# Kernel tuning notes

Measured on AMD Instinct MI355X. Metric: run time of the kernel, lower is better.

## Reference

```python
import jax, jax.numpy as jnp
import numpy as np


def setup_inputs() -> dict:
    key = jax.random.key(0)
    k1, k2, k3, k4 = jax.random.split(key, 4)
    B, C, H, W = 8, 64, 64, 64
    Ck = C // 8  # query/key channels
    x = jax.random.normal(k1, (B, C, H, W), dtype=jnp.float32)
    # 1x1 conv1d weights (bias=False); spectral norm only rescales the weight,
    # so plain matrices are math-equivalent at a given parameter value.
    wq = jax.random.normal(k2, (Ck, C), dtype=jnp.float32) * (1.0 / np.sqrt(C))
    wk = jax.random.normal(k3, (Ck, C), dtype=jnp.float32) * (1.0 / np.sqrt(C))
    wv = jax.random.normal(k4, (C, C), dtype=jnp.float32) * (1.0 / np.sqrt(C))
    gamma = jnp.array([0.5], dtype=jnp.float32)  # nonzero so attention path is exercised
    return {"x": x, "wq": wq, "wk": wk, "wv": wv, "gamma": gamma}


def reference(x, wq, wk, wv, gamma):
    B, C, H, W = x.shape
    xf = x.reshape(B, C, H * W)                      # [B, C, N]
    f = jnp.einsum('kc,bcn->bkn', wq, xf)            # [B, C/8, N]
    g = jnp.einsum('kc,bcn->bkn', wk, xf)            # [B, C/8, N]
    h = jnp.einsum('oc,bcn->bon', wv, xf)            # [B, C,   N]
    scores = jnp.einsum('bkn,bkm->bnm', f, g)        # f^T g, [B, N, N]
    beta = jax.nn.softmax(scores, axis=1)            # softmax over dim=1 (rows), as in torch
    o = jnp.einsum('bcn,bnm->bcm', h, beta)          # [B, C, N]
    out = gamma[0] * o + xf
    return out.reshape(B, C, H, W)
```

## Files before the change

### kernel.cpp

```cpp
#include <hip/hip_runtime.h>
#include <hip/hip_bf16.h>

typedef __bf16 bf16x8 __attribute__((ext_vector_type(8)));
typedef float f32x4 __attribute__((ext_vector_type(4)));
typedef float f32x16 __attribute__((ext_vector_type(16)));
typedef unsigned int uint2v __attribute__((ext_vector_type(2)));

#define MFMA16 __builtin_amdgcn_mfma_f32_16x16x32_bf16
#define MFMA32 __builtin_amdgcn_mfma_f32_32x32x16_bf16

__device__ __forceinline__ unsigned short f2b(float f) {
  unsigned int u = __float_as_uint(f);
  u += 0x7FFFu + ((u >> 16) & 1u);
  return (unsigned short)(u >> 16);
}

__device__ __forceinline__ float b2f(unsigned short s) {
  return __uint_as_float(((unsigned)s) << 16);
}

union U128 {
  uint4 u;
  unsigned short s[8];
  bf16x8 b;
};

union BPack {
  __hip_bfloat162 h2;
  unsigned u;
};

__device__ __forceinline__ unsigned packbf(float a, float b) {
  BPack p;
  p.h2 = __float22bfloat162_rn(make_float2(a, b));
  return p.u;
}

__global__ __launch_bounds__(256, 2) void proj_kernel(
    const float* __restrict__ x, const float* __restrict__ wq,
    const float* __restrict__ wk, const float* __restrict__ wv_w,
    unsigned short* __restrict__ f_t, unsigned short* __restrict__ g_t,
    unsigned short* __restrict__ h_out) {
  __shared__ unsigned short xT[64 * 64];
  __shared__ unsigned short wT[96 * 72];
  __shared__ unsigned short hT[64 * 72];

  const int tid = (int)threadIdx.x;
  const int wvp = tid >> 6;
  const int lane = tid & 63;
  const int b = (int)blockIdx.x & 7;
  const int n0 = ((int)blockIdx.x >> 3) << 6;

  {
    const float* xb = x + ((size_t)b << 18) + n0 + lane;
    const int c0 = wvp * 16;
    float xv[16];
#pragma unroll
    for (int cc = 0; cc < 16; ++cc) xv[cc] = xb[(size_t)(c0 + cc) << 12];
#pragma unroll
    for (int p = 0; p < 4; ++p) {
      const int c = c0 + 4 * p;
      uint2 d;
      d.x = packbf(xv[4 * p + 0], xv[4 * p + 1]);
      d.y = packbf(xv[4 * p + 2], xv[4 * p + 3]);
      const int g = c >> 3;
      const int idx = lane * 64 + (((g ^ (lane & 7)) << 3) | (((c >> 2) & 1) << 2));
      *(uint2*)&xT[idx] = d;
    }
  }
#pragma unroll
  for (int i = 0; i < 20; ++i) {
    const int idx = i * 256 + tid;
    const float wval = (idx < 512) ? wq[idx] * 1.44269504f
                     : (idx < 1024) ? wk[idx - 512]
                                    : wv_w[idx - 1024];
    wT[(idx >> 6) * 72 + (idx & 63)] = f2b(wval);
  }
  __syncthreads();

  const int t = lane & 15, q = lane >> 4;
  const int nloc = wvp * 16 + t;
  U128 Bf[2];
#pragma unroll
  for (int kp = 0; kp < 2; ++kp) {
    const int g = kp * 4 + q;
    Bf[kp].u = *(const uint4*)&xT[nloc * 64 + ((g ^ (nloc & 7)) << 3)];
  }
  const int nabs = n0 + nloc;

  {
    f32x4 acc = {0.f, 0.f, 0.f, 0.f};
#pragma unroll
    for (int kp = 0; kp < 2; ++kp) {
      U128 Af;
      Af.u = *(const uint4*)&wT[t * 72 + ((kp * 4 + q) << 3)];
      acc = MFMA16(Af.b, Bf[kp].b, acc, 0, 0, 0);
    }
    uint2 d;
    d.x = packbf(acc[0], acc[1]);
    d.y = packbf(acc[2], acc[3]);
    unsigned short* dst = (q & 2) ? g_t : f_t;
    *(uint2*)&dst[((size_t)((b << 12) + nabs) << 3) + ((q & 1) << 2)] = d;
  }
#pragma unroll
  for (int rt = 1; rt < 5; ++rt) {
    f32x4 acc = {0.f, 0.f, 0.f, 0.f};
#pragma unroll
    for (int kp = 0; kp < 2; ++kp) {
      U128 Af;
      Af.u = *(const uint4*)&wT[(rt * 16 + t) * 72 + ((kp * 4 + q) << 3)];
      acc = MFMA16(Af.b, Bf[kp].b, acc, 0, 0, 0);
    }
    const int cbase = (rt - 1) * 16 + 4 * q;
#pragma unroll
    for (int reg = 0; reg < 4; ++reg)
      hT[(cbase + reg) * 72 + nloc] = f2b(acc[reg]);
  }
  __syncthreads();

  {
    const int hc = tid & 63;
    const int hw = tid >> 6;
    const uint4 v0 = *(const uint4*)&hT[hc * 72 + hw * 16];
    const uint4 v1 = *(const uint4*)&hT[hc * 72 + hw * 16 + 8];
    const size_t hbase =
        ((size_t)b << 18) + ((size_t)((n0 + hw * 16) >> 3) << 9) + (hc << 3);
    *(uint4*)&h_out[hbase] = v0;
    *(uint4*)&h_out[hbase + 512] = v1;
  }
}

__global__ __launch_bounds__(256, 2) void attn_kernel(
    const unsigned short* __restrict__ f_t, const unsigned short* __restrict__ g_t,
    const unsigned short* __restrict__ h, const float* __restrict__ x,
    const float* __restrict__ gamma, float* __restrict__ out) {
  __shared__ unsigned short Opart[4][32][66];
  __shared__ float lred[4][64];
  __shared__ float lsum[64];

  const int tid = (int)threadIdx.x;
  const int wave = tid >> 6;
  const int lane = tid & 63;
  const int ml = lane & 31;
  const int hh = lane >> 5;

  const int b = (int)blockIdx.x & 7;
  const int m0 = ((int)blockIdx.x >> 3) << 6;

  const unsigned short* fb = f_t + ((size_t)b << 15);
  const unsigned short* hb = h + ((size_t)b << 18);

  U128 G0, G1;
  G0.u = make_uint4(0u, 0u, 0u, 0u);
  G1.u = make_uint4(0u, 0u, 0u, 0u);
  if (hh == 0) {
    G0.u = *(const uint4*)(g_t + ((size_t)((b << 12) + m0 + ml) << 3));
    G1.u = *(const uint4*)(g_t + ((size_t)((b << 12) + m0 + 32 + ml) << 3));
  }

  f32x16 O00 = {}, O01 = {}, O10 = {}, O11 = {};
  float2 lp0v = make_float2(0.f, 0.f), lp1v = make_float2(0.f, 0.f);
  const f32x16 ZC = {};

  const int nbase = wave << 10;

  const unsigned short* fp = fb + ((size_t)(nbase + ml) << 3);
  const unsigned short* hp = hb + ((nbase >> 3) << 9) + (hh << 9) + (ml << 3);

  U128 F0, F1, Ha_e[4], Ha_o[4];
  f32x16 S0, S1;

  F0.u = *(const uint4*)(fp);
  F1.u = *(const uint4*)(fp + 256);
  Ha_e[0].u = *(const uint4*)(hp);
  Ha_e[1].u = *(const uint4*)(hp + 256);
  Ha_e[2].u = *(const uint4*)(hp + 1024);
  Ha_e[3].u = *(const uint4*)(hp + 1280);
  S0 = MFMA32(F0.b, G0.b, ZC, 0, 0, 0);
  S1 = MFMA32(F0.b, G1.b, ZC, 0, 0, 0);

  auto half = [&](f32x16& S, const U128& G, float2& lp, f32x16& Oa, f32x16& Ob,
                  const U128* Hv, const U128& Fn, bool produce) {
    float e[16];
#pragma unroll
    for (int r = 0; r < 16; ++r) e[r] = __builtin_amdgcn_exp2f(S[r]);
    if (produce) S = MFMA32(Fn.b, G.b, ZC, 0, 0, 0);
    lp.x += ((e[0] + e[2]) + (e[4] + e[6])) + ((e[8] + e[10]) + (e[12] + e[14]));
    lp.y += ((e[1] + e[3]) + (e[5] + e[7])) + ((e[9] + e[11]) + (e[13] + e[15]));
#pragma unroll
    for (int kt = 0; kt < 2; ++kt) {
      const unsigned A0 = packbf(e[8 * kt + 0], e[8 * kt + 1]);
      const unsigned A1 = packbf(e[8 * kt + 2], e[8 * kt + 3]);
      const unsigned B0 = packbf(e[8 * kt + 4], e[8 * kt + 5]);
      const unsigned B1 = packbf(e[8 * kt + 6], e[8 * kt + 7]);
      const uint2v r0 = __builtin_amdgcn_permlane32_swap(A0, B0, false, false);
      const uint2v r1 = __builtin_amdgcn_permlane32_swap(A1, B1, false, false);
      U128 P;
      P.u.x = r0[0];
      P.u.y = r1[0];
      P.u.z = r0[1];
      P.u.w = r1[1];
      Oa = MFMA32(Hv[2 * kt + 0].b, P.b, Oa, 0, 0, 0);
      Ob = MFMA32(Hv[2 * kt + 1].b, P.b, Ob, 0, 0, 0);
    }
  };
  auto body = [&](const U128* Hv, const U128& Fn, bool produce) {
    half(S0, G0, lp0v, O00, O01, Hv, Fn, produce);
    half(S1, G1, lp1v, O10, O11, Hv, Fn, produce);
  };

#pragma unroll 1
  for (int j = 0; j < 15; ++j) {
    Ha_o[0].u = *(const uint4*)(hp + 2048);
    Ha_o[1].u = *(const uint4*)(hp + 2304);
    Ha_o[2].u = *(const uint4*)(hp + 3072);
    Ha_o[3].u = *(const uint4*)(hp + 3328);
    F0.u = *(const uint4*)(fp + 512);
    body(Ha_e, F1, true);
    hp += 4096;
    Ha_e[0].u = *(const uint4*)(hp);
    Ha_e[1].u = *(const uint4*)(hp + 256);
    Ha_e[2].u = *(const uint4*)(hp + 1024);
    Ha_e[3].u = *(const uint4*)(hp + 1280);
    F1.u = *(const uint4*)(fp + 768);
    body(Ha_o, F0, true);
    fp += 512;
  }
  Ha_o[0].u = *(const uint4*)(hp + 2048);
  Ha_o[1].u = *(const uint4*)(hp + 2304);
  Ha_o[2].u = *(const uint4*)(hp + 3072);
  Ha_o[3].u = *(const uint4*)(hp + 3328);
  body(Ha_e, F1, true);
  body(Ha_o, F1, false);

  float lp0 = lp0v.x + lp0v.y;
  float lp1 = lp1v.x + lp1v.y;
  lp0 += __shfl_xor(lp0, 32, 64);
  lp1 += __shfl_xor(lp1, 32, 64);
  if (hh == 0) {
    lred[wave][ml] = lp0;
    lred[wave][32 + ml] = lp1;
  }

  const float gam = gamma[0];

  auto stash = [&](const f32x16& Oa, const f32x16& Ob) {
#pragma unroll
    for (int r = 0; r < 8; ++r) {
      const int c0 = ((2 * r) & 3) + 8 * (r >> 1) + 4 * hh;
      *(unsigned*)&Opart[wave][ml][c0] = packbf(Oa[2 * r], Oa[2 * r + 1]);
      *(unsigned*)&Opart[wave][ml][c0 + 32] = packbf(Ob[2 * r], Ob[2 * r + 1]);
    }
  };
  auto drain = [&](int p) {
    const int c = tid >> 2;
    const int m8 = (tid & 3) << 3;
    float a[8];
#pragma unroll
    for (int j = 0; j < 8; ++j) a[j] = 0.f;
#pragma unroll
    for (int w = 0; w < 4; ++w)
#pragma unroll
      for (int j = 0; j < 8; ++j) a[j] += b2f(Opart[w][m8 + j][c]);
    const f32x4 l0 = *(const f32x4*)&lsum[p * 32 + m8];
    const f32x4 l1 = *(const f32x4*)&lsum[p * 32 + m8 + 4];
    const size_t oi = (((size_t)b * 64 + c) << 12) + m0 + p * 32 + m8;
    f32x4 xo0 = *(const f32x4*)(x + oi);
    f32x4 xo1 = *(const f32x4*)(x + oi + 4);
#pragma unroll
    for (int j = 0; j < 4; ++j) {
      xo0[j] += gam / l0[j] * a[j];
      xo1[j] += gam / l1[j] * a[j + 4];
    }
    *(f32x4*)(out + oi) = xo0;
    *(f32x4*)(out + oi + 4) = xo1;
  };

  stash(O00, O01);
  __syncthreads();
  if (tid < 64)
    lsum[tid] = (lred[0][tid] + lred[1][tid]) + (lred[2][tid] + lred[3][tid]);
  __syncthreads();
  drain(0);
  __syncthreads();
  stash(O10, O11);
  __syncthreads();
  drain(1);
}

extern "C" void kernel_launch(void* const* d_in, const int* in_sizes, int n_in,
                              void* d_out, int out_size, void* d_ws, size_t ws_size,
                              hipStream_t stream) {
  (void)in_sizes; (void)n_in; (void)out_size; (void)ws_size;
  const float* x = (const float*)d_in[0];
  const float* wq = (const float*)d_in[1];
  const float* wk = (const float*)d_in[2];
  const float* wv = (const float*)d_in[3];
  const float* gamma = (const float*)d_in[4];
  float* out = (float*)d_out;

  unsigned short* f_t = (unsigned short*)d_ws;
  unsigned short* g_t = f_t + (size_t)8 * 4096 * 8;
  unsigned short* h = g_t + (size_t)8 * 4096 * 8;

  proj_kernel<<<512, 256, 0, stream>>>(x, wq, wk, wv, f_t, g_t, h);
  attn_kernel<<<512, 256, 0, stream>>>(f_t, g_t, h, x, gamma, out);
}
```

Before: 100.5 us.

## Fuse projection and attention kernels with a software grid barrier

Merges the projection kernel and the attention kernel into one persistent launch. A global atomic-counter barrier, reset by a memset before launch, separates the two phases, and the shared memory of both phases is overlaid through a union. This removes the second kernel launch and its inter-kernel gap. It relies on all 512 blocks being co-resident, which needs 2 blocks per CU on 256 CUs, and the spin-wait has a guard that could let blocks proceed early and read stale data. It also adds a memset call.

```diff
diff --git a/kernel.cpp b/kernel.cpp
--- a/kernel.cpp
+++ b/kernel.cpp
@@ -36,256 +36,285 @@
   return p.u;
 }
 
-__global__ __launch_bounds__(256, 2) void proj_kernel(
+__device__ __forceinline__ void grid_barrier(unsigned* bar, unsigned nblk) {
+  __syncthreads();
+  if (threadIdx.x == 0) {
+    __threadfence();
+    atomicAdd(bar, 1u);
+    unsigned v;
+    int guard = 0;
+    do {
+      v = __hip_atomic_load(bar, __ATOMIC_RELAXED, __HIP_MEMORY_SCOPE_AGENT);
+    } while (v < nblk && ++guard < (1 << 27));
+    __threadfence();
+  }
+  __syncthreads();
+}
+
+__global__ __launch_bounds__(256, 2) void fused_kernel(
     const float* __restrict__ x, const float* __restrict__ wq,
     const float* __restrict__ wk, const float* __restrict__ wv_w,
     unsigned short* __restrict__ f_t, unsigned short* __restrict__ g_t,
-    unsigned short* __restrict__ h_out) {
-  __shared__ unsigned short xT[64 * 64];
-  __shared__ unsigned short wT[96 * 72];
-  __shared__ unsigned short hT[64 * 72];
+    unsigned short* __restrict__ h, const float* __restrict__ gamma,
+    float* __restrict__ out, unsigned* __restrict__ bar) {
+  __shared__ union SMem {
+    struct {
+      unsigned short xT[64 * 64];
+      unsigned short wT[96 * 72];
+      unsigned short hT[64 * 72];
+    } p;
+    struct {
+      unsigned short Opart[4][32][66];
+      float lred[4][64];
+      float lsum[64];
+    } a;
+  } sm;
 
   const int tid = (int)threadIdx.x;
-  const int wvp = tid >> 6;
-  const int lane = tid & 63;
   const int b = (int)blockIdx.x & 7;
-  const int n0 = ((int)blockIdx.x >> 3) << 6;
+  const int t64 = (int)blockIdx.x >> 3;
 
   {
-    const float* xb = x + ((size_t)b << 18) + n0 + lane;
-    const int c0 = wvp * 16;
-    float xv[16];
-#pragma unroll
-    for (int cc = 0; cc < 16; ++cc) xv[cc] = xb[(size_t)(c0 + cc) << 12];
-#pragma unroll
-    for (int p = 0; p < 4; ++p) {
-      const int c = c0 + 4 * p;
+    const int wvp = tid >> 6;
+    const int lane = tid & 63;
+    const int n0 = t64 << 6;
+
+    {
+      const float* xb = x + ((size_t)b << 18) + n0 + lane;
+      const int c0 = wvp * 16;
+      float xv[16];
+#pragma unroll
+      for (int cc = 0; cc < 16; ++cc) xv[cc] = xb[(size_t)(c0 + cc) << 12];
+#pragma unroll
+      for (int p = 0; p < 4; ++p) {
+        const int c = c0 + 4 * p;
+        uint2 d;
+        d.x = packbf(xv[4 * p + 0], xv[4 * p + 1]);
+        d.y = packbf(xv[4 * p + 2], xv[4 * p + 3]);
+        const int g = c >> 3;
+        const int idx =
+            lane * 64 + (((g ^ (lane & 7)) << 3) | (((c >> 2) & 1) << 2));
+        *(uint2*)&sm.p.xT[idx] = d;
+      }
+    }
+#pragma unroll
+    for (int i = 0; i < 20; ++i) {
+      const int idx = i * 256 + tid;
+      const float wval = (idx < 512) ? wq[idx] * 1.44269504f
+                       : (idx < 1024) ? wk[idx - 512]
+                                      : wv_w[idx - 1024];
+      sm.p.wT[(idx >> 6) * 72 + (idx & 63)] = f2b(wval);
+    }
+    __syncthreads();
+
+    const int t = lane & 15, q = lane >> 4;
+    const int nloc = wvp * 16 + t;
+    U128 Bf[2];
+#pragma unroll
+    for (int kp = 0; kp < 2; ++kp) {
+      const int g = kp * 4 + q;
+      Bf[kp].u = *(const uint4*)&sm.p.xT[nloc * 64 + ((g ^ (nloc & 7)) << 3)];
+    }
+    const int nabs = n0 + nloc;
+
+    {
+      f32x4 acc = {0.f, 0.f, 0.f, 0.f};
+#pragma unroll
+      for (int kp = 0; kp < 2; ++kp) {
+        U128 Af;
+        Af.u = *(const uint4*)&sm.p.wT[t * 72 + ((kp * 4 + q) << 3)];
+        acc = MFMA16(Af.b, Bf[kp].b, acc, 0, 0, 0);
+      }
       uint2 d;
-      d.x = packbf(xv[4 * p + 0], xv[4 * p + 1]);
-      d.y = packbf(xv[4 * p + 2], xv[4 * p + 3]);
-      const int g = c >> 3;
-      const int idx = lane * 64 + (((g ^ (lane & 7)) << 3) | (((c >> 2) & 1) << 2));
-      *(uint2*)&xT[idx] = d;
+      d.x = packbf(acc[0], acc[1]);
+      d.y = packbf(acc[2], acc[3]);
+      unsigned short* dst = (q & 2) ? g_t : f_t;
+      *(uint2*)&dst[((size_t)((b << 12) + nabs) << 3) + ((q & 1) << 2)] = d;
+    }
+#pragma unroll
+    for (int rt = 1; rt < 5; ++rt) {
+      f32x4 acc = {0.f, 0.f, 0.f, 0.f};
+#pragma unroll
+      for (int kp = 0; kp < 2; ++kp) {
+        U128 Af;
+        Af.u = *(const uint4*)&sm.p.wT[(rt * 16 + t) * 72 + ((kp * 4 + q) << 3)];
+        acc = MFMA16(Af.b, Bf[kp].b, acc, 0, 0, 0);
+      }
+      const int cbase = (rt - 1) * 16 + 4 * q;
+#pragma unroll
+      for (int reg = 0; reg < 4; ++reg)
+        sm.p.hT[(cbase + reg) * 72 + nloc] = f2b(acc[reg]);
+    }
+    __syncthreads();
+
+    {
+      const int hc = tid & 63;
+      const int hw = tid >> 6;
+      const uint4 v0 = *(const uint4*)&sm.p.hT[hc * 72 + hw * 16];
+      const uint4 v1 = *(const uint4*)&sm.p.hT[hc * 72 + hw * 16 + 8];
+      const size_t hbase =
+          ((size_t)b << 18) + ((size_t)((n0 + hw * 16) >> 3) << 9) + (hc << 3);
+      *(uint4*)&h[hbase] = v0;
+      *(uint4*)&h[hbase + 512] = v1;
     }
   }
-#pragma unroll
-  for (int i = 0; i < 20; ++i) {
-    const int idx = i * 256 + tid;
-    const float wval = (idx < 512) ? wq[idx] * 1.44269504f
-                     : (idx < 1024) ? wk[idx - 512]
-                                    : wv_w[idx - 1024];
-    wT[(idx >> 6) * 72 + (idx & 63)] = f2b(wval);
-  }
-  __syncthreads();
-
-  const int t = lane & 15, q = lane >> 4;
-  const int nloc = wvp * 16 + t;
-  U128 Bf[2];
-#pragma unroll
-  for (int kp = 0; kp < 2; ++kp) {
-    const int g = kp * 4 + q;
-    Bf[kp].u = *(const uint4*)&xT[nloc * 64 + ((g ^ (nloc & 7)) << 3)];
-  }
-  const int nabs = n0 + nloc;
+
+  grid_barrier(bar, (unsigned)gridDim.x);
 
   {
-    f32x4 acc = {0.f, 0.f, 0.f, 0.f};
-#pragma unroll
-    for (int kp = 0; kp < 2; ++kp) {
-      U128 Af;
-      Af.u = *(const uint4*)&wT[t * 72 + ((kp * 4 + q) << 3)];
-      acc = MFMA16(Af.b, Bf[kp].b, acc, 0, 0, 0);
-    }
-    uint2 d;
-    d.x = packbf(acc[0], acc[1]);
-    d.y = packbf(acc[2], acc[3]);
-    unsigned short* dst = (q & 2) ? g_t : f_t;
-    *(uint2*)&dst[((size_t)((b << 12) + nabs) << 3) + ((q & 1) << 2)] = d;
-  }
-#pragma unroll
-  for (int rt = 1; rt < 5; ++rt) {
-    f32x4 acc = {0.f, 0.f, 0.f, 0.f};
-#pragma unroll
-    for (int kp = 0; kp < 2; ++kp) {
-      U128 Af;
-      Af.u = *(const uint4*)&wT[(rt * 16 + t) * 72 + ((kp * 4 + q) << 3)];
-      acc = MFMA16(Af.b, Bf[kp].b, acc, 0, 0, 0);
-    }
-    const int cbase = (rt - 1) * 16 + 4 * q;
-#pragma unroll
-    for (int reg = 0; reg < 4; ++reg)
-      hT[(cbase + reg) * 72 + nloc] = f2b(acc[reg]);
-  }
-  __syncthreads();
-
-  {
-    const int hc = tid & 63;
-    const int hw = tid >> 6;
-    const uint4 v0 = *(const uint4*)&hT[hc * 72 + hw * 16];
-    const uint4 v1 = *(const uint4*)&hT[hc * 72 + hw * 16 + 8];
-    const size_t hbase =
-        ((size_t)b << 18) + ((size_t)((n0 + hw * 16) >> 3) << 9) + (hc << 3);
-    *(uint4*)&h_out[hbase] = v0;
-    *(uint4*)&h_out[hbase + 512] = v1;
-  }
-}
-
-__global__ __launch_bounds__(256, 2) void attn_kernel(
-    const unsigned short* __restrict__ f_t, const unsigned short* __restrict__ g_t,
-    const unsigned short* __restrict__ h, const float* __restrict__ x,
-    const float* __restrict__ gamma, float* __restrict__ out) {
-  __shared__ unsigned short Opart[4][32][66];
-  __shared__ float lred[4][64];
-  __shared__ float lsum[64];
-
-  const int tid = (int)threadIdx.x;
-  const int wave = tid >> 6;
-  const int lane = tid & 63;
-  const int ml = lane & 31;
-  const int hh = lane >> 5;
-
-  const int b = (int)blockIdx.x & 7;
-  const int m0 = ((int)blockIdx.x >> 3) << 6;
-
-  const unsigned short* fb = f_t + ((size_t)b << 15);
-  const unsigned short* hb = h + ((size_t)b << 18);
-
-  U128 G0, G1;
-  G0.u = make_uint4(0u, 0u, 0u, 0u);
-  G1.u = make_uint4(0u, 0u, 0u, 0u);
-  if (hh == 0) {
-    G0.u = *(const uint4*)(g_t + ((size_t)((b << 12) + m0 + ml) << 3));
-    G1.u = *(const uint4*)(g_t + ((size_t)((b << 12) + m0 + 32 + ml) << 3));
-  }
-
-  f32x16 O00 = {}, O01 = {}, O10 = {}, O11 = {};
-  float2 lp0v = make_float2(0.f, 0.f), lp1v = make_float2(0.f, 0.f);
-  const f32x16 ZC = {};
-
-  const int nbase = wave << 10;
-
-  const unsigned short* fp = fb + ((size_t)(nbase + ml) << 3);
-  const unsigned short* hp = hb + ((nbase >> 3) << 9) + (hh << 9) + (ml << 3);
-
-  U128 F0, F1, Ha_e[4], Ha_o[4];
-  f32x16 S0, S1;
-
-  F0.u = *(const uint4*)(fp);
-  F1.u = *(const uint4*)(fp + 256);
-  Ha_e[0].u = *(const uint4*)(hp);
-  Ha_e[1].u = *(const uint4*)(hp + 256);
-  Ha_e[2].u = *(const uint4*)(hp + 1024);
-  Ha_e[3].u = *(const uint4*)(hp + 1280);
-  S0 = MFMA32(F0.b, G0.b, ZC, 0, 0, 0);
-  S1 = MFMA32(F0.b, G1.b, ZC, 0, 0, 0);
-
-  auto half = [&](f32x16& S, const U128& G, float2& lp, f32x16& Oa, f32x16& Ob,
-                  const U128* Hv, const U128& Fn, bool produce) {
-    float e[16];
-#pragma unroll
-    for (int r = 0; r < 16; ++r) e[r] = __builtin_amdgcn_exp2f(S[r]);
-    if (produce) S = MFMA32(Fn.b, G.b, ZC, 0, 0, 0);
-    lp.x += ((e[0] + e[2]) + (e[4] + e[6])) + ((e[8] + e[10]) + (e[12] + e[14]));
-    lp.y += ((e[1] + e[3]) + (e[5] + e[7])) + ((e[9] + e[11]) + (e[13] + e[15]));
-#pragma unroll
-    for (int kt = 0; kt < 2; ++kt) {
-      const unsigned A0 = packbf(e[8 * kt + 0], e[8 * kt + 1]);
-      const unsigned A1 = packbf(e[8 * kt + 2], e[8 * kt + 3]);
-      const unsigned B0 = packbf(e[8 * kt + 4], e[8 * kt + 5]);
-      const unsigned B1 = packbf(e[8 * kt + 6], e[8 * kt + 7]);
-      const uint2v r0 = __builtin_amdgcn_permlane32_swap(A0, B0, false, false);
-      const uint2v r1 = __builtin_amdgcn_permlane32_swap(A1, B1, false, false);
-      U128 P;
-      P.u.x = r0[0];
-      P.u.y = r1[0];
-      P.u.z = r0[1];
-      P.u.w = r1[1];
-      Oa = MFMA32(Hv[2 * kt + 0].b, P.b, Oa, 0, 0, 0);
-      Ob = MFMA32(Hv[2 * kt + 1].b, P.b, Ob, 0, 0, 0);
-    }
-  };
-  auto body = [&](const U128* Hv, const U128& Fn, bool produce) {
-    half(S0, G0, lp0v, O00, O01, Hv, Fn, produce);
-    half(S1, G1, lp1v, O10, O11, Hv, Fn, produce);
-  };
+    const int wave = tid >> 6;
+    const int lane = tid & 63;
+    const int ml = lane & 31;
+    const int hh = lane >> 5;
+    const int m0 = t64 << 6;
+
+    const unsigned short* fb = f_t + ((size_t)b << 15);
+    const unsigned short* hb = h + ((size_t)b << 18);
+
+    U128 G0, G1;
+    G0.u = make_uint4(0u, 0u, 0u, 0u);
+    G1.u = make_uint4(0u, 0u, 0u, 0u);
+    if (hh == 0) {
+      G0.u = *(const uint4*)(g_t + ((size_t)((b << 12) + m0 + ml) << 3));
+      G1.u = *(const uint4*)(g_t + ((size_t)((b << 12) + m0 + 32 + ml) << 3));
+    }
+
+    f32x16 O00 = {}, O01 = {}, O10 = {}, O11 = {};
+    float2 lp0v = make_float2(0.f, 0.f), lp1v = make_float2(0.f, 0.f);
+    const f32x16 ZC = {};
+
+    const int nbase = wave << 10;
+
+    const unsigned short* fp = fb + ((size_t)(nbase + ml) << 3);
+    const unsigned short* hp =
+        hb + ((nbase >> 3) << 9) + (hh << 9) + (ml << 3);
+
+    U128 F0, F1, Ha_e[4], Ha_o[4];
+    f32x16 S0, S1;
+
+    F0.u = *(const uint4*)(fp);
+    F1.u = *(const uint4*)(fp + 256);
+    Ha_e[0].u = *(const uint4*)(hp);
+    Ha_e[1].u = *(const uint4*)(hp + 256);
+    Ha_e[2].u = *(const uint4*)(hp + 1024);
+    Ha_e[3].u = *(const uint4*)(hp + 1280);
+    S0 = MFMA32(F0.b, G0.b, ZC, 0, 0, 0);
+    S1 = MFMA32(F0.b, G1.b, ZC, 0, 0, 0);
+
+    auto half = [&](f32x16& S, const U128& G, float2& lp, f32x16& Oa,
+                    f32x16& Ob, const U128* Hv, const U128& Fn, bool produce) {
+      float e[16];
+#pragma unroll
+      for (int r = 0; r < 16; ++r) e[r] = __builtin_amdgcn_exp2f(S[r]);
+      if (produce) S = MFMA32(Fn.b, G.b, ZC, 0, 0, 0);
+      lp.x +=
+          ((e[0] + e[2]) + (e[4] + e[6])) + ((e[8] + e[10]) + (e[12] + e[14]));
+      lp.y +=
+          ((e[1] + e[3]) + (e[5] + e[7])) + ((e[9] + e[11]) + (e[13] + e[15]));
+#pragma unroll
+      for (int kt = 0; kt < 2; ++kt) {
+        const unsigned A0 = packbf(e[8 * kt + 0], e[8 * kt + 1]);
+        const unsigned A1 = packbf(e[8 * kt + 2], e[8 * kt + 3]);
+        const unsigned B0 = packbf(e[8 * kt + 4], e[8 * kt + 5]);
+        const unsigned B1 = packbf(e[8 * kt + 6], e[8 * kt + 7]);
+        const uint2v r0 = __builtin_amdgcn_permlane32_swap(A0, B0, false, false);
+        const uint2v r1 = __builtin_amdgcn_permlane32_swap(A1, B1, false, false);
+        U128 P;
+        P.u.x = r0[0];
+        P.u.y = r1[0];
+        P.u.z = r0[1];
+        P.u.w = r1[1];
+        Oa = MFMA32(Hv[2 * kt + 0].b, P.b, Oa, 0, 0, 0);
+        Ob = MFMA32(Hv[2 * kt + 1].b, P.b, Ob, 0, 0, 0);
+      }
+    };
+    auto body = [&](const U128* Hv, const U128& Fn, bool produce) {
+      half(S0, G0, lp0v, O00, O01, Hv, Fn, produce);
+      half(S1, G1, lp1v, O10, O11, Hv, Fn, produce);
+    };
 
 #pragma unroll 1
-  for (int j = 0; j < 15; ++j) {
+    for (int j = 0; j < 15; ++j) {
+      Ha_o[0].u = *(const uint4*)(hp + 2048);
+      Ha_o[1].u = *(const uint4*)(hp + 2304);
+      Ha_o[2].u = *(const uint4*)(hp + 3072);
+      Ha_o[3].u = *(const uint4*)(hp + 3328);
+      F0.u = *(const uint4*)(fp + 512);
+      body(Ha_e, F1, true);
+      hp += 4096;
+      Ha_e[0].u = *(const uint4*)(hp);
+      Ha_e[1].u = *(const uint4*)(hp + 256);
+      Ha_e[2].u = *(const uint4*)(hp + 1024);
+      Ha_e[3].u = *(const uint4*)(hp + 1280);
+      F1.u = *(const uint4*)(fp + 768);
+      body(Ha_o, F0, true);
+      fp += 512;
+    }
     Ha_o[0].u = *(const uint4*)(hp + 2048);
     Ha_o[1].u = *(const uint4*)(hp + 2304);
     Ha_o[2].u = *(const uint4*)(hp + 3072);
     Ha_o[3].u = *(const uint4*)(hp + 3328);
-    F0.u = *(const uint4*)(fp + 512);
     body(Ha_e, F1, true);
-    hp += 4096;
-    Ha_e[0].u = *(const uint4*)(hp);
-    Ha_e[1].u = *(const uint4*)(hp + 256);
-    Ha_e[2].u = *(const uint4*)(hp + 1024);
-    Ha_e[3].u = *(const uint4*)(hp + 1280);
-    F1.u = *(const uint4*)(fp + 768);
-    body(Ha_o, F0, true);
-    fp += 512;
+    body(Ha_o, F1, false);
+
+    float lp0 = lp0v.x + lp0v.y;
+    float lp1 = lp1v.x + lp1v.y;
+    lp0 += __shfl_xor(lp0, 32, 64);
+    lp1 += __shfl_xor(lp1, 32, 64);
+
+    __syncthreads();
+    if (hh == 0) {
+      sm.a.lred[wave][ml] = lp0;
+      sm.a.lred[wave][32 + ml] = lp1;
+    }
+
+    const float gam = gamma[0];
+
+    auto stash = [&](const f32x16& Oa, const f32x16& Ob) {
+#pragma unroll
+      for (int r = 0; r < 8; ++r) {
+        const int c0 = ((2 * r) & 3) + 8 * (r >> 1) + 4 * hh;
+        *(unsigned*)&sm.a.Opart[wave][ml][c0] = packbf(Oa[2 * r], Oa[2 * r + 1]);
+        *(unsigned*)&sm.a.Opart[wave][ml][c0 + 32] =
+            packbf(Ob[2 * r], Ob[2 * r + 1]);
+      }
+    };
+    auto drain = [&](int p) {
+      const int c = tid >> 2;
+      const int m8 = (tid & 3) << 3;
+      float a[8];
+#pragma unroll
+      for (int j = 0; j < 8; ++j) a[j] = 0.f;
+#pragma unroll
+      for (int w = 0; w < 4; ++w)
+#pragma unroll
+        for (int j = 0; j < 8; ++j) a[j] += b2f(sm.a.Opart[w][m8 + j][c]);
+      const f32x4 l0 = *(const f32x4*)&sm.a.lsum[p * 32 + m8];
+      const f32x4 l1 = *(const f32x4*)&sm.a.lsum[p * 32 + m8 + 4];
+      const size_t oi = (((size_t)b * 64 + c) << 12) + m0 + p * 32 + m8;
+      f32x4 xo0 = *(const f32x4*)(x + oi);
+      f32x4 xo1 = *(const f32x4*)(x + oi + 4);
+#pragma unroll
+      for (int j = 0; j < 4; ++j) {
+        xo0[j] += gam / l0[j] * a[j];
+        xo1[j] += gam / l1[j] * a[j + 4];
+      }
+      *(f32x4*)(out + oi) = xo0;
+      *(f32x4*)(out + oi + 4) = xo1;
+    };
+
+    stash(O00, O01);
+    __syncthreads();
+    if (tid < 64)
+      sm.a.lsum[tid] = (sm.a.lred[0][tid] + sm.a.lred[1][tid]) +
+                       (sm.a.lred[2][tid] + sm.a.lred[3][tid]);
+    __syncthreads();
+    drain(0);
+    __syncthreads();
+    stash(O10, O11);
+    __syncthreads();
+    drain(1);
   }
-  Ha_o[0].u = *(const uint4*)(hp + 2048);
-  Ha_o[1].u = *(const uint4*)(hp + 2304);
-  Ha_o[2].u = *(const uint4*)(hp + 3072);
-  Ha_o[3].u = *(const uint4*)(hp + 3328);
-  body(Ha_e, F1, true);
-  body(Ha_o, F1, false);
-
-  float lp0 = lp0v.x + lp0v.y;
-  float lp1 = lp1v.x + lp1v.y;
-  lp0 += __shfl_xor(lp0, 32, 64);
-  lp1 += __shfl_xor(lp1, 32, 64);
-  if (hh == 0) {
-    lred[wave][ml] = lp0;
-    lred[wave][32 + ml] = lp1;
-  }
-
-  const float gam = gamma[0];
-
-  auto stash = [&](const f32x16& Oa, const f32x16& Ob) {
-#pragma unroll
-    for (int r = 0; r < 8; ++r) {
-      const int c0 = ((2 * r) & 3) + 8 * (r >> 1) + 4 * hh;
-      *(unsigned*)&Opart[wave][ml][c0] = packbf(Oa[2 * r], Oa[2 * r + 1]);
-      *(unsigned*)&Opart[wave][ml][c0 + 32] = packbf(Ob[2 * r], Ob[2 * r + 1]);
-    }
-  };
-  auto drain = [&](int p) {
-    const int c = tid >> 2;
-    const int m8 = (tid & 3) << 3;
-    float a[8];
-#pragma unroll
-    for (int j = 0; j < 8; ++j) a[j] = 0.f;
-#pragma unroll
-    for (int w = 0; w < 4; ++w)
-#pragma unroll
-      for (int j = 0; j < 8; ++j) a[j] += b2f(Opart[w][m8 + j][c]);
-    const f32x4 l0 = *(const f32x4*)&lsum[p * 32 + m8];
-    const f32x4 l1 = *(const f32x4*)&lsum[p * 32 + m8 + 4];
-    const size_t oi = (((size_t)b * 64 + c) << 12) + m0 + p * 32 + m8;
-    f32x4 xo0 = *(const f32x4*)(x + oi);
-    f32x4 xo1 = *(const f32x4*)(x + oi + 4);
-#pragma unroll
-    for (int j = 0; j < 4; ++j) {
-      xo0[j] += gam / l0[j] * a[j];
-      xo1[j] += gam / l1[j] * a[j + 4];
-    }
-    *(f32x4*)(out + oi) = xo0;
-    *(f32x4*)(out + oi + 4) = xo1;
-  };
-
-  stash(O00, O01);
-  __syncthreads();
-  if (tid < 64)
-    lsum[tid] = (lred[0][tid] + lred[1][tid]) + (lred[2][tid] + lred[3][tid]);
-  __syncthreads();
-  drain(0);
-  __syncthreads();
-  stash(O10, O11);
-  __syncthreads();
-  drain(1);
 }
 
 extern "C" void kernel_launch(void* const* d_in, const int* in_sizes, int n_in,
@@ -302,7 +331,9 @@
   unsigned short* f_t = (unsigned short*)d_ws;
   unsigned short* g_t = f_t + (size_t)8 * 4096 * 8;
   unsigned short* h = g_t + (size_t)8 * 4096 * 8;
-
-  proj_kernel<<<512, 256, 0, stream>>>(x, wq, wk, wv, f_t, g_t, h);
-  attn_kernel<<<512, 256, 0, stream>>>(f_t, g_t, h, x, gamma, out);
-}
+  unsigned* bar = (unsigned*)(h + (size_t)8 * 512 * 64 * 8);
+
+  hipMemsetAsync(bar, 0, 16, stream);
+  fused_kernel<<<512, 256, 0, stream>>>(x, wq, wk, wv, f_t, g_t, h, gamma,
+                                        out, bar);
+}
```

Measured after the change: 151.3 us. 50.5% more time.
